# Optimization experiments

Hardware: AMD Instinct MI355X
Metric: run time of the kernel (lower is better)

The kernel has to match this reference:

```python
import jax, jax.numpy as jnp
import numpy as np

N = 16384      # nodes
E = 262144     # edges (avg degree 16)
R = 9          # relation types
D_IN = 384     # embed_size
D_H = 768      # hidden_size
N_CLASSES = 5


def setup_inputs() -> dict:
    key = jax.random.key(0)
    ks = jax.random.split(key, 11)
    s = 0.02
    return {
        "x": jax.random.normal(ks[0], (N, D_IN), jnp.float32),
        "edge_index": jax.random.randint(ks[1], (2, E), 0, N, dtype=jnp.int64)
        if jax.config.jax_enable_x64 else jax.random.randint(ks[1], (2, E), 0, N).astype(jnp.int32),
        "edge_type": jax.random.randint(ks[2], (E,), 0, R).astype(jnp.int32),
        "rel_W": jax.random.normal(ks[3], (R, D_H, D_IN), jnp.float32) * s,
        "rel_b": jax.random.normal(ks[4], (R, D_H), jnp.float32) * s,
        "norm_constants": jnp.ones((R,), jnp.float32),
        "mp_lin_W": jax.random.normal(ks[5], (D_H, D_H), jnp.float32) * s,
        "mp_lin_b": jax.random.normal(ks[6], (D_H,), jnp.float32) * s,
        "mp_self_W": jax.random.normal(ks[7], (D_H, D_H), jnp.float32) * s,
        "mp_self_b": jax.random.normal(ks[8], (D_H,), jnp.float32) * s,
        "out_W": jax.random.normal(ks[9], (N_CLASSES, D_H), jnp.float32) * s,
        "out_b": jax.random.normal(ks[10], (N_CLASSES,), jnp.float32) * s,
    }


def reference(x, edge_index, edge_type, rel_W, rel_b, norm_constants,
              mp_lin_W, mp_lin_b, mp_self_W, mp_self_b, out_W, out_b):
    n = x.shape[0]
    src = edge_index[0]  # j : message source (x_j)
    dst = edge_index[1]  # i : aggregation target

    # --- RelationAwareMP ---
    # edge_weights[i, j] from x @ x.T, computed per edge (identical math)
    ew = jnp.einsum('ed,ed->e', x[dst], x[src])                  # [E]
    norm = ew / norm_constants[edge_type]                        # [E]
    # per-relation linear applied to all nodes, then gathered per edge
    h = jnp.einsum('nd,rhd->rnh', x, rel_W) + rel_b[:, None, :]  # [R,N,H]
    msg = h[edge_type, src]                                      # [E,H]
    aggr = jax.ops.segment_sum(norm[:, None] * msg, dst, num_segments=n)
    x1 = jax.nn.relu(aggr)                                       # [N,H]

    # --- MP (add aggregation + self transform) ---
    self_x = x1 @ mp_self_W.T + mp_self_b
    hm = x1 @ mp_lin_W.T + mp_lin_b
    aggr2 = jax.ops.segment_sum(hm[src], dst, num_segments=n)
    x2 = jax.nn.relu(aggr2 + self_x)                             # [N,H]

    # --- readout ---
    pooled = x2.mean(axis=0)                                     # [H]
    return pooled @ out_W.T + out_b                              # [N_CLASSES]
```

## Files before the change

### kernel.cpp

```cpp
#include <hip/hip_runtime.h>

typedef unsigned char  u8;
typedef unsigned short u16;
typedef unsigned int   u32;

#define NN   16384
#define EE   262144
#define RR   9
#define DIN  384
#define DH   768
#define KSU  3456
#define KS   3488

typedef float  f32x4 __attribute__((ext_vector_type(4)));
typedef float  f32x2 __attribute__((ext_vector_type(2)));
typedef __bf16 b16x8 __attribute__((ext_vector_type(8)));

__device__ __forceinline__ u16 f2bf(float f){
  u32 u = __builtin_bit_cast(u32, f);
  u += 0x7fffu + ((u >> 16) & 1u);
  return (u16)(u >> 16);
}
__device__ __forceinline__ float bf2f(u16 h){
  u32 u = ((u32)h) << 16;
  return __builtin_bit_cast(float, u);
}
__device__ __forceinline__ float bflo(u32 u){ return __builtin_bit_cast(float, u << 16); }
__device__ __forceinline__ float bfhi(u32 u){ return __builtin_bit_cast(float, u & 0xffff0000u); }
__device__ __forceinline__ u32 pk2(float a, float b){
  return (u32)f2bf(a) | ((u32)f2bf(b) << 16);
}
__device__ __forceinline__ void gll16(const void* g, void* l){
  __builtin_amdgcn_global_load_lds((const __attribute__((address_space(1))) void*)g,
                                   (__attribute__((address_space(3))) void*)l, 16, 0, 0);
}

__global__ void k_count(const int* __restrict__ dst, int* __restrict__ counts){
  const int e = blockIdx.x*256 + threadIdx.x;
  if (e < EE) atomicAdd(&counts[dst[e]], 1);
}

__global__ __launch_bounds__(1024) void k_scan(const int* __restrict__ counts,
                                               int* __restrict__ starts,
                                               int* __restrict__ cursor){
  __shared__ int tot[1024];
  const int t = threadIdx.x;
  int loc[16]; int s = 0;
  #pragma unroll
  for (int j=0;j<16;j++){ loc[j] = counts[t*16+j]; s += loc[j]; }
  tot[t] = s;
  __syncthreads();
  for (int o=1;o<1024;o<<=1){
    int v = (t>=o) ? tot[t-o] : 0;
    __syncthreads();
    tot[t] += v;
    __syncthreads();
  }
  int run = tot[t] - s;
  #pragma unroll
  for (int j=0;j<16;j++){ starts[t*16+j] = run; cursor[t*16+j] = run; run += loc[j]; }
  if (t == 1023) starts[NN] = run;
}

__global__ void k_place(const int* __restrict__ src, const int* __restrict__ dst,
                        const int* __restrict__ et, int* __restrict__ cursor,
                        int* __restrict__ srcp, int* __restrict__ dstp,
                        int* __restrict__ rp){
  const int e = blockIdx.x*256 + threadIdx.x;
  if (e < EE){
    const int p = atomicAdd(&cursor[dst[e]], 1);
    srcp[p] = src[e];
    dstp[p] = dst[e];
    rp[p]   = et[e];
  }
}

__global__ void k_convX(const float* __restrict__ x, u32* __restrict__ xb){
  const int idx = blockIdx.x*256 + threadIdx.x;
  const f32x2 v = ((const f32x2*)x)[idx];
  xb[idx] = pk2(v.x, v.y);
}

__global__ void k_convW1(const float* __restrict__ rW, const float* __restrict__ rb,
                         u16* __restrict__ Wst){
  const int hh = blockIdx.y;
  const int k  = blockIdx.x*256 + threadIdx.x;
  if (k >= KS) return;
  float v;
  if (k < KSU){ const int r = k / DIN; const int d = k - r*DIN;
                v = rW[((long)r*DH + hh)*DIN + d]; }
  else if (k < KSU + RR){ const int r = k - KSU; v = rb[(long)r*DH + hh]; }
  else v = 0.f;
  Wst[(long)hh*KS + k] = f2bf(v);
}

__global__ void k_convW2(const float* __restrict__ lW, const float* __restrict__ sW,
                         u16* __restrict__ WB){
  const int idx = blockIdx.x*256 + threadIdx.x;
  const float v = (idx < DH*DH) ? lW[idx] : sW[idx - DH*DH];
  WB[idx] = f2bf(v);
}

__global__ __launch_bounds__(256, 4) void k_dots(const u32* __restrict__ xb,
                                                 const int* __restrict__ srcp,
                                                 const int* __restrict__ dstp,
                                                 const int* __restrict__ rp,
                                                 const float* __restrict__ nc,
                                                 float* __restrict__ normp){
  const int p = blockIdx.x*4 + (threadIdx.x >> 6);
  const int l = threadIdx.x & 63;
  const u32* xs = xb + (long)srcp[p]*192;
  const u32* xd = xb + (long)dstp[p]*192;
  float s = 0.f;
  #pragma unroll
  for (int j=0;j<3;j++){
    const u32 a = xs[l + 64*j], b = xd[l + 64*j];
    s += bflo(a)*bflo(b) + bfhi(a)*bfhi(b);
  }
  #pragma unroll
  for (int o=32;o;o>>=1) s += __shfl_xor(s, o);
  if (l == 0) normp[p] = s / nc[rp[p]];
}

__global__ __launch_bounds__(256, 3) void k_phase1f(const u32* __restrict__ xb,
                                                    const int* __restrict__ srcp,
                                                    const int* __restrict__ rp,
                                                    const float* __restrict__ normp,
                                                    const int* __restrict__ starts,
                                                    u16* __restrict__ s){
  const int w = threadIdx.x >> 6, l = threadIdx.x & 63;
  const int i = blockIdx.x*4 + w;
  float acc[RR][6];
  float cacc[RR];
  #pragma unroll
  for (int r=0;r<RR;r++){
    cacc[r] = 0.f;
    #pragma unroll
    for (int j=0;j<6;j++) acc[r][j] = 0.f;
  }
  const int e0 = starts[i], np = starts[i+1] - e0;

  u32 A0=0,A1=0,A2=0,B0=0,B1=0,B2=0,C0=0,C1=0,C2=0;
  float nA=0.f,nB=0.f,nC=0.f; int Ar=0,Br=0,Cr=0;

  #define LOADSLOT(S0,S1,S2,NR,RV,idx) { \
    const u32* xs_ = xb + (long)srcp[idx]*192; \
    S0 = xs_[l]; S1 = xs_[64+l]; S2 = xs_[128+l]; \
    NR = normp[idx]; RV = rp[idx]; }
  #define CONSUME(S0,S1,S2,NR,RV) { \
    const float f0=bflo(S0), f1=bfhi(S0), f2=bflo(S1), \
                f3=bfhi(S1), f4=bflo(S2), f5=bfhi(S2); \
    const float nm = NR; \
    switch (RV){ \
      case 0: cacc[0]+=nm; acc[0][0]+=nm*f0; acc[0][1]+=nm*f1; acc[0][2]+=nm*f2; acc[0][3]+=nm*f3; acc[0][4]+=nm*f4; acc[0][5]+=nm*f5; break; \
      case 1: cacc[1]+=nm; acc[1][0]+=nm*f0; acc[1][1]+=nm*f1; acc[1][2]+=nm*f2; acc[1][3]+=nm*f3; acc[1][4]+=nm*f4; acc[1][5]+=nm*f5; break; \
      case 2: cacc[2]+=nm; acc[2][0]+=nm*f0; acc[2][1]+=nm*f1; acc[2][2]+=nm*f2; acc[2][3]+=nm*f3; acc[2][4]+=nm*f4; acc[2][5]+=nm*f5; break; \
      case 3: cacc[3]+=nm; acc[3][0]+=nm*f0; acc[3][1]+=nm*f1; acc[3][2]+=nm*f2; acc[3][3]+=nm*f3; acc[3][4]+=nm*f4; acc[3][5]+=nm*f5; break; \
      case 4: cacc[4]+=nm; acc[4][0]+=nm*f0; acc[4][1]+=nm*f1; acc[4][2]+=nm*f2; acc[4][3]+=nm*f3; acc[4][4]+=nm*f4; acc[4][5]+=nm*f5; break; \
      case 5: cacc[5]+=nm; acc[5][0]+=nm*f0; acc[5][1]+=nm*f1; acc[5][2]+=nm*f2; acc[5][3]+=nm*f3; acc[5][4]+=nm*f4; acc[5][5]+=nm*f5; break; \
      case 6: cacc[6]+=nm; acc[6][0]+=nm*f0; acc[6][1]+=nm*f1; acc[6][2]+=nm*f2; acc[6][3]+=nm*f3; acc[6][4]+=nm*f4; acc[6][5]+=nm*f5; break; \
      case 7: cacc[7]+=nm; acc[7][0]+=nm*f0; acc[7][1]+=nm*f1; acc[7][2]+=nm*f2; acc[7][3]+=nm*f3; acc[7][4]+=nm*f4; acc[7][5]+=nm*f5; break; \
      default:cacc[8]+=nm; acc[8][0]+=nm*f0; acc[8][1]+=nm*f1; acc[8][2]+=nm*f2; acc[8][3]+=nm*f3; acc[8][4]+=nm*f4; acc[8][5]+=nm*f5; break; \
    } }

  if (np > 0) LOADSLOT(A0,A1,A2,nA,Ar,e0)
  if (np > 1) LOADSLOT(B0,B1,B2,nB,Br,e0+1)
  if (np > 2) LOADSLOT(C0,C1,C2,nC,Cr,e0+2)

  for (int p=0; p<np; p+=3){
    CONSUME(A0,A1,A2,nA,Ar)
    if (p+3 < np) LOADSLOT(A0,A1,A2,nA,Ar,e0+p+3)
    if (p+1 < np){
      CONSUME(B0,B1,B2,nB,Br)
      if (p+4 < np) LOADSLOT(B0,B1,B2,nB,Br,e0+p+4)
    }
    if (p+2 < np){
      CONSUME(C0,C1,C2,nC,Cr)
      if (p+5 < np) LOADSLOT(C0,C1,C2,nC,Cr,e0+p+5)
    }
  }
  #undef CONSUME
  #undef LOADSLOT

  u16* srow = s + (long)i*KS;
  #pragma unroll
  for (int r=0;r<RR;r++){
    #pragma unroll
    for (int seg=0;seg<3;seg++)
      ((u32*)(srow + r*DIN + seg*128))[l] = pk2(acc[r][seg*2], acc[r][seg*2+1]);
  }
  float cv = 0.f;
  #pragma unroll
  for (int r=0;r<RR;r++) cv = (l == r) ? cacc[r] : cv;
  if (l < 32) srow[KSU + l] = f2bf(l < RR ? cv : 0.f);
}

template<int MODE>
__global__ __launch_bounds__(256, 2)
void k_gemm_bt(const u16* __restrict__ A, const u16* __restrict__ B,
               int M, int N, int K,
               u16* __restrict__ O0, u16* __restrict__ O1,
               const float* __restrict__ b0, const float* __restrict__ b1)
{
  __shared__ __align__(16) u16 As[128*32];
  __shared__ __align__(16) u16 Bs[128*32];
  const int t  = threadIdx.x;
  const int wv = t >> 6;
  const int ln = t & 63;
  const int wm = wv >> 1, wn = wv & 1;
  const long m0 = (long)blockIdx.x * 128;
  const long n0 = (long)blockIdx.y * 128;

  const int srow  = ln >> 2;
  const int skcol = (ln & 3) * 8;

  f32x4 acc[4][4];
  #pragma unroll
  for (int i=0;i<4;i++)
    #pragma unroll
    for (int j=0;j<4;j++) acc[i][j] = {0.f,0.f,0.f,0.f};

  const int fr = ln & 15, fq = ln >> 4;
  const int nk = K >> 5;
  for (int kb=0; kb<nk; ++kb){
    const long k0 = (long)kb * 32;
    #pragma unroll
    for (int q=0;q<2;q++){
      const int seg = wv*2 + q;
      const int row = seg*16 + srow;
      gll16(A + (m0 + row)*(long)K + k0 + skcol, &As[seg*512]);
      gll16(B + (n0 + row)*(long)K + k0 + skcol, &Bs[seg*512]);
    }
    __syncthreads();
    b16x8 av[4], bv[4];
    #pragma unroll
    for (int i=0;i<4;i++){
      av[i] = *(const b16x8*)&As[(wm*64 + i*16 + fr)*32 + fq*8];
      bv[i] = *(const b16x8*)&Bs[(wn*64 + i*16 + fr)*32 + fq*8];
    }
    #pragma unroll
    for (int i=0;i<4;i++)
      #pragma unroll
      for (int j=0;j<4;j++)
        acc[i][j] = __builtin_amdgcn_mfma_f32_16x16x32_bf16(av[i], bv[j], acc[i][j], 0, 0, 0);
    __syncthreads();
  }

  #pragma unroll
  for (int i=0;i<4;i++){
    #pragma unroll
    for (int j=0;j<4;j++){
      #pragma unroll
      for (int r=0;r<4;r++){
        const long m = m0 + wm*64 + i*16 + fq*4 + r;
        const long n = n0 + wn*64 + j*16 + fr;
        float v = acc[i][j][r];
        if (MODE == 0){
          v = v > 0.f ? v : 0.f;
          O0[m*DH + n] = f2bf(v);
        } else {
          if (n < DH) O0[m*DH + n]      = f2bf(v + b0[n]);
          else        O1[m*DH + (n-DH)] = f2bf(v + b1[n-DH]);
        }
      }
    }
  }
}

__global__ __launch_bounds__(256, 4) void k_phase2(const u32* __restrict__ hm32,
                                                   const u32* __restrict__ sfx32,
                                                   const int* __restrict__ srcp,
                                                   const int* __restrict__ starts,
                                                   float* __restrict__ pooled8){
  const int w = threadIdx.x >> 6, l = threadIdx.x & 63;
  const int t = threadIdx.x;
  __shared__ float pl[DH];
  #pragma unroll
  for (int k=0;k<3;k++) pl[t + 256*k] = 0.f;
  __syncthreads();

  float po[12];
  #pragma unroll
  for (int j=0;j<12;j++) po[j] = 0.f;

  for (int q=0;q<2;q++){
    const int i = blockIdx.x*8 + w*2 + q;
    float a[12];
    #pragma unroll
    for (int j=0;j<12;j++) a[j] = 0.f;
    const int e0 = starts[i], np = starts[i+1] - e0;

    u32 A0=0,A1=0,A2=0,A3=0,A4=0,A5=0;
    u32 B0=0,B1=0,B2=0,B3=0,B4=0,B5=0;
    if (np > 0){
      const u32* hr = hm32 + (long)srcp[e0]*384;
      A0=hr[l]; A1=hr[64+l]; A2=hr[128+l]; A3=hr[192+l]; A4=hr[256+l]; A5=hr[320+l];
    }
    if (np > 1){
      const u32* hr = hm32 + (long)srcp[e0+1]*384;
      B0=hr[l]; B1=hr[64+l]; B2=hr[128+l]; B3=hr[192+l]; B4=hr[256+l]; B5=hr[320+l];
    }
    for (int p=0; p<np; p+=2){
      a[0]+=bflo(A0); a[1]+=bfhi(A0); a[2]+=bflo(A1); a[3] +=bfhi(A1);
      a[4]+=bflo(A2); a[5]+=bfhi(A2); a[6] +=bflo(A3); a[7] +=bfhi(A3);
      a[8]+=bflo(A4); a[9]+=bfhi(A4); a[10]+=bflo(A5); a[11]+=bfhi(A5);
      if (p+2 < np){
        const u32* hr = hm32 + (long)srcp[e0+p+2]*384;
        A0=hr[l]; A1=hr[64+l]; A2=hr[128+l]; A3=hr[192+l]; A4=hr[256+l]; A5=hr[320+l];
      }
      if (p+1 < np){
        a[0]+=bflo(B0); a[1]+=bfhi(B0); a[2] +=bflo(B1); a[3] +=bfhi(B1);
        a[4]+=bflo(B2); a[5]+=bfhi(B2); a[6] +=bflo(B3); a[7] +=bfhi(B3);
        a[8]+=bflo(B4); a[9]+=bfhi(B4); a[10]+=bflo(B5); a[11]+=bfhi(B5);
        if (p+3 < np){
          const u32* hr = hm32 + (long)srcp[e0+p+3]*384;
          B0=hr[l]; B1=hr[64+l]; B2=hr[128+l]; B3=hr[192+l]; B4=hr[256+l]; B5=hr[320+l];
        }
      }
    }
    const u32* sr = sfx32 + (long)i*384;
    #pragma unroll
    for (int j=0;j<6;j++){
      const u32 sv = sr[l + 64*j];
      float v0 = a[2*j]   + bflo(sv);
      float v1 = a[2*j+1] + bfhi(sv);
      po[2*j]   += v0 > 0.f ? v0 : 0.f;
      po[2*j+1] += v1 > 0.f ? v1 : 0.f;
    }
  }
  #pragma unroll
  for (int j=0;j<6;j++){
    atomicAdd(&pl[2*l   + 128*j], po[2*j]);
    atomicAdd(&pl[2*l+1 + 128*j], po[2*j+1]);
  }
  __syncthreads();
  float* pd = pooled8 + (blockIdx.x & 7)*DH;
  #pragma unroll
  for (int k=0;k<3;k++) atomicAdd(&pd[t + 256*k], pl[t + 256*k]);
}

__global__ __launch_bounds__(256) void k_final(const float* __restrict__ pooled8,
                                               const float* __restrict__ oW,
                                               const float* __restrict__ ob,
                                               float* __restrict__ out){
  __shared__ float ps[DH];
  __shared__ float red[256];
  const int t = threadIdx.x;
  for (int h=t; h<DH; h+=256){
    float s = 0.f;
    #pragma unroll
    for (int c=0;c<8;c++) s += pooled8[c*DH + h];
    ps[h] = s;
  }
  __syncthreads();
  for (int c=0;c<5;c++){
    float p = 0.f;
    for (int h=t; h<DH; h+=256) p += ps[h]*oW[c*DH + h];
    red[t] = p; __syncthreads();
    for (int o=128;o;o>>=1){ if (t<o) red[t]+=red[t+o]; __syncthreads(); }
    if (t == 0) out[c] = red[0]*(1.f/(float)NN) + ob[c];
    __syncthreads();
  }
}

extern "C" void kernel_launch(void* const* d_in, const int* in_sizes, int n_in,
                              void* d_out, int out_size, void* d_ws, size_t ws_size,
                              hipStream_t stream)
{
  (void)in_sizes; (void)n_in; (void)out_size; (void)ws_size;
  const float* x     = (const float*)d_in[0];
  const int*   ei    = (const int*)  d_in[1];
  const int*   et    = (const int*)  d_in[2];
  const float* relW  = (const float*)d_in[3];
  const float* relb  = (const float*)d_in[4];
  const float* nc    = (const float*)d_in[5];
  const float* linW  = (const float*)d_in[6];
  const float* linb  = (const float*)d_in[7];
  const float* selfW = (const float*)d_in[8];
  const float* selfb = (const float*)d_in[9];
  const float* outW  = (const float*)d_in[10];
  const float* outb  = (const float*)d_in[11];
  float* out = (float*)d_out;

  u8* w = (u8*)d_ws;
  int*   counts  = (int*)(w + 0);
  int*   starts  = (int*)(w + 65536);
  int*   cursor  = (int*)(w + 131328);
  int*   srcp    = (int*)(w + 196864);
  int*   dstp    = (int*)(w + 1245440);
  int*   rp      = (int*)(w + 2294016);
  float* normp   = (float*)(w + 3342592);
  u16*   Wst     = (u16*)(w + 4391168);
  u16*   WB      = (u16*)(w + 9748736);
  u16*   x1      = (u16*)(w + 12108032);
  u32*   xb      = (u32*)x1;
  float* pooled8 = (float*)(w + 37273856);
  u16*   S       = (u16*)(w + 37298432);
  u16*   hm      = S;
  u16*   sfx     = (u16*)(w + 37298432 + 25165824);

  const int* esrc = ei;
  const int* edst = ei + EE;

  hipMemsetAsync(counts, 0, NN*sizeof(int), stream);
  hipMemsetAsync(pooled8, 0, 8*DH*sizeof(float), stream);

  k_count <<<EE/256, 256, 0, stream>>>(edst, counts);
  k_scan  <<<1, 1024, 0, stream>>>(counts, starts, cursor);
  k_place <<<EE/256, 256, 0, stream>>>(esrc, edst, et, cursor, srcp, dstp, rp);
  k_convX <<<(NN*DIN/2)/256, 256, 0, stream>>>(x, xb);
  k_convW1<<<dim3(14, DH), 256, 0, stream>>>(relW, relb, Wst);
  k_convW2<<<(2*DH*DH)/256, 256, 0, stream>>>(linW, selfW, WB);
  k_dots  <<<EE/4, 256, 0, stream>>>(xb, srcp, dstp, rp, nc, normp);
  k_phase1f<<<NN/4, 256, 0, stream>>>(xb, srcp, rp, normp, starts, S);
  k_gemm_bt<0><<<dim3(NN/128, DH/128), 256, 0, stream>>>(
      S, Wst, NN, DH, KS, x1, (u16*)nullptr, (const float*)nullptr, (const float*)nullptr);
  k_gemm_bt<1><<<dim3(NN/128, 2*DH/128), 256, 0, stream>>>(
      x1, WB, NN, 2*DH, DH, hm, sfx, linb, selfb);
  k_phase2<<<NN/8, 256, 0, stream>>>((const u32*)hm, (const u32*)sfx, srcp, starts, pooled8);
  k_final <<<1, 256, 0, stream>>>(pooled8, outW, outb, out);
}
```

Before: 545.6 us.

## Merge conversion kernels into one launch and swizzle GEMM LDS tiles

Replaces the three separate fp32-to-bf16 conversion kernels with a single flat-indexed kernel, removing two launches. It also applies an XOR-like rotation of the 8-element k-chunk within each LDS row in the bf16 GEMM, on both the global-to-LDS copy and the fragment reads, to reduce LDS bank conflicts. The merged kernel adds 64-bit division per element for the weight section, and the swizzle adds a little address arithmetic.

Measured after the change: 542.7 us. Within noise of the previous version (-0.5%).

```diff
diff --git a/kernel.cpp b/kernel.cpp
--- a/kernel.cpp
+++ b/kernel.cpp
@@ -75,30 +75,38 @@
   }
 }
 
-__global__ void k_convX(const float* __restrict__ x, u32* __restrict__ xb){
-  const int idx = blockIdx.x*256 + threadIdx.x;
-  const f32x2 v = ((const f32x2*)x)[idx];
-  xb[idx] = pk2(v.x, v.y);
-}
-
-__global__ void k_convW1(const float* __restrict__ rW, const float* __restrict__ rb,
-                         u16* __restrict__ Wst){
-  const int hh = blockIdx.y;
-  const int k  = blockIdx.x*256 + threadIdx.x;
-  if (k >= KS) return;
-  float v;
-  if (k < KSU){ const int r = k / DIN; const int d = k - r*DIN;
-                v = rW[((long)r*DH + hh)*DIN + d]; }
-  else if (k < KSU + RR){ const int r = k - KSU; v = rb[(long)r*DH + hh]; }
-  else v = 0.f;
-  Wst[(long)hh*KS + k] = f2bf(v);
-}
-
-__global__ void k_convW2(const float* __restrict__ lW, const float* __restrict__ sW,
-                         u16* __restrict__ WB){
-  const int idx = blockIdx.x*256 + threadIdx.x;
-  const float v = (idx < DH*DH) ? lW[idx] : sW[idx - DH*DH];
-  WB[idx] = f2bf(v);
+#define NXP (NN*DIN/2)
+#define NW1 (DH*KS)
+#define NW2 (2*DH*DH)
+__global__ __launch_bounds__(256) void k_conv(const float* __restrict__ x,
+                                              const float* __restrict__ rW,
+                                              const float* __restrict__ rb,
+                                              const float* __restrict__ lW,
+                                              const float* __restrict__ sW,
+                                              u32* __restrict__ xb,
+                                              u16* __restrict__ Wst,
+                                              u16* __restrict__ WB){
+  long j = (long)blockIdx.x*256 + threadIdx.x;
+  if (j < NXP){
+    const f32x2 v = ((const f32x2*)x)[j];
+    xb[j] = pk2(v.x, v.y);
+    return;
+  }
+  j -= NXP;
+  if (j < NW1){
+    const int hh = (int)(j / KS);
+    const int k  = (int)(j - (long)hh*KS);
+    float v;
+    if (k < KSU){ const int r = k / DIN; const int d = k - r*DIN;
+                  v = rW[((long)r*DH + hh)*DIN + d]; }
+    else if (k < KSU + RR){ const int r = k - KSU; v = rb[(long)r*DH + hh]; }
+    else v = 0.f;
+    Wst[(long)hh*KS + k] = f2bf(v);
+    return;
+  }
+  j -= NW1;
+  const float v = (j < DH*DH) ? lW[j] : sW[j - DH*DH];
+  WB[j] = f2bf(v);
 }
 
 __global__ __launch_bounds__(256, 4) void k_dots(const u32* __restrict__ xb,
@@ -211,8 +219,9 @@
   const long m0 = (long)blockIdx.x * 128;
   const long n0 = (long)blockIdx.y * 128;
 
-  const int srow  = ln >> 2;
-  const int skcol = (ln & 3) * 8;
+  const int ri    = ln >> 2;
+  const int kw    = (ri + (ri >> 2)) & 3;
+  const int skcol = (((ln & 3) - kw) & 3) * 8;
 
   f32x4 acc[4][4];
   #pragma unroll
@@ -221,13 +230,15 @@
     for (int j=0;j<4;j++) acc[i][j] = {0.f,0.f,0.f,0.f};
 
   const int fr = ln & 15, fq = ln >> 4;
+  const int kr    = (fr + (fr >> 2)) & 3;
+  const int rdoff = ((fq + kr) & 3) * 8;
   const int nk = K >> 5;
   for (int kb=0; kb<nk; ++kb){
     const long k0 = (long)kb * 32;
     #pragma unroll
     for (int q=0;q<2;q++){
       const int seg = wv*2 + q;
-      const int row = seg*16 + srow;
+      const int row = seg*16 + ri;
       gll16(A + (m0 + row)*(long)K + k0 + skcol, &As[seg*512]);
       gll16(B + (n0 + row)*(long)K + k0 + skcol, &Bs[seg*512]);
     }
@@ -235,8 +246,8 @@
     b16x8 av[4], bv[4];
     #pragma unroll
     for (int i=0;i<4;i++){
-      av[i] = *(const b16x8*)&As[(wm*64 + i*16 + fr)*32 + fq*8];
-      bv[i] = *(const b16x8*)&Bs[(wn*64 + i*16 + fr)*32 + fq*8];
+      av[i] = *(const b16x8*)&As[(wm*64 + i*16 + fr)*32 + rdoff];
+      bv[i] = *(const b16x8*)&Bs[(wn*64 + i*16 + fr)*32 + rdoff];
     }
     #pragma unroll
     for (int i=0;i<4;i++)
@@ -408,9 +419,8 @@
   k_count <<<EE/256, 256, 0, stream>>>(edst, counts);
   k_scan  <<<1, 1024, 0, stream>>>(counts, starts, cursor);
   k_place <<<EE/256, 256, 0, stream>>>(esrc, edst, et, cursor, srcp, dstp, rp);
-  k_convX <<<(NN*DIN/2)/256, 256, 0, stream>>>(x, xb);
-  k_convW1<<<dim3(14, DH), 256, 0, stream>>>(relW, relb, Wst);
-  k_convW2<<<(2*DH*DH)/256, 256, 0, stream>>>(linW, selfW, WB);
+  k_conv  <<<(NXP + NW1 + NW2)/256, 256, 0, stream>>>(x, relW, relb, linW, selfW,
+                                                      xb, Wst, WB);
   k_dots  <<<EE/4, 256, 0, stream>>>(xb, srcp, dstp, rp, nc, normp);
   k_phase1f<<<NN/4, 256, 0, stream>>>(xb, srcp, rp, normp, starts, S);
   k_gemm_bt<0><<<dim3(NN/128, DH/128), 256, 0, stream>>>(
```
